# Optimization experiments

Measured on AMD Instinct MI355X. Metric: run time of the kernel, lower is better.

Reference implementation:

```python
import jax, jax.numpy as jnp
import numpy as np

L = 64          # latent_gcn == latent2_gcn == latent_linear
N = 8           # coarse_size (forward hardcodes eye(8))
NEG = 0.2       # LeakyReLU slope
EPS = 1e-5      # BatchNorm1d eps


def _bn(v, g, b):
    # training-mode BatchNorm1d over the node axis (axis=-2), per (B,C) instance
    m = v.mean(axis=-2, keepdims=True)
    var = ((v - m) ** 2).mean(axis=-2, keepdims=True)  # biased, as torch BN
    return (v - m) / jnp.sqrt(var + EPS) * g + b


def _path(A, W1, b1, W2, b2, Wm, bm, gm, betam, Ws, bs, gs, betas, noise):
    # A: [B, c, 8, 8] row-normalized adjacency. x = eye(8) so support1 = W1.
    x1 = jax.nn.leaky_relu(A @ W1 + b1, NEG)            # [B,c,8,L]
    x2 = jax.nn.leaky_relu(A @ (x1 @ W2) + b2, NEG)     # [B,c,8,L]
    mean = _bn(x2 @ Wm + bm, gm, betam)
    logvar = _bn(x2 @ Ws + bs, gs, betas)
    return mean + jnp.exp(0.5 * logvar) * noise         # reparameterization


def setup_inputs() -> dict:
    key = jax.random.key(0)
    ks = jax.random.split(key, 40)
    B, C = 2048, 32
    d = {
        "adj": jax.random.uniform(ks[0], (B, C, N, N), jnp.float32),
        "noise": jax.random.normal(ks[1], (N, L), jnp.float32),
    }
    i = 2
    for p in ("p", "n"):
        shapes = [
            (f"W1_{p}", (N, L)), (f"b1_{p}", (L,)),
            (f"W2_{p}", (L, L)), (f"b2_{p}", (L,)),
            (f"Wm_{p}", (L, L)), (f"bm_{p}", (L,)), (f"gm_{p}", (L,)), (f"betam_{p}", (L,)),
            (f"Ws_{p}", (L, L)), (f"bs_{p}", (L,)), (f"gs_{p}", (L,)), (f"betas_{p}", (L,)),
        ]
        for name, sh in shapes:
            if name.startswith("beta"):
                d[name] = jnp.zeros(sh, jnp.float32)
            elif name.startswith("g"):
                d[name] = jnp.ones(sh, jnp.float32)
            else:
                stdv = 1.0 / float(np.sqrt(sh[-1]))
                d[name] = jax.random.uniform(ks[i], sh, jnp.float32, -stdv, stdv)
                i += 1
    return d


def reference(adj, noise,
              W1_p, b1_p, W2_p, b2_p, Wm_p, bm_p, gm_p, betam_p, Ws_p, bs_p, gs_p, betas_p,
              W1_n, b1_n, W2_n, b2_n, Wm_n, bm_n, gm_n, betam_n, Ws_n, bs_n, gs_n, betas_n):
    # row-normalize each 8x8 adjacency (pygcn-style normalize)
    s = adj.sum(axis=-1, keepdims=True)
    A = adj / jnp.where(s == 0, 1.0, s)
    out_p = _path(A[:, :1], W1_p, b1_p, W2_p, b2_p, Wm_p, bm_p, gm_p, betam_p,
                  Ws_p, bs_p, gs_p, betas_p, noise)          # ii == 0
    out_n = _path(A[:, 1:], W1_n, b1_n, W2_n, b2_n, Wm_n, bm_n, gm_n, betam_n,
                  Ws_n, bs_n, gs_n, betas_n, noise)          # ii >= 1
    return jnp.concatenate([out_p, out_n], axis=1)           # [B, C, 8, L]
```

## Files before the change

### kernel.cpp

```cpp
#include <hip/hip_runtime.h>

typedef float v4f __attribute__((ext_vector_type(4)));
typedef short v8s __attribute__((ext_vector_type(8)));
typedef v8s v8s_a __attribute__((may_alias));

#define PBLOCKS 256
#define NEG 0.2f

static __device__ __forceinline__ void split8(const float* e, v8s& hi, v8s& lo) {
  union U { v8s s; unsigned u[4]; } H, L;
#pragma unroll
  for (int j = 0; j < 4; ++j) {
    union { float f; unsigned u; } e0, e1, h0, h1, l0, l1;
    e0.f = e[2 * j]; e1.f = e[2 * j + 1];
    H.u[j] = __builtin_amdgcn_perm(e1.u, e0.u, 0x07060302u);
    h0.u = e0.u & 0xFFFF0000u; h1.u = e1.u & 0xFFFF0000u;
    l0.f = e0.f - h0.f; l1.f = e1.f - h1.f;
    L.u[j] = __builtin_amdgcn_perm(l1.u, l0.u, 0x07060302u);
  }
  hi = H.s; lo = L.s;
}

static __device__ __forceinline__ v8s rne8(const float* e) {
  union U { v8s s; unsigned u[4]; } H;
#pragma unroll
  for (int j = 0; j < 4; ++j) {
    union { float f; unsigned u; } e0, e1;
    e0.f = e[2 * j]; e1.f = e[2 * j + 1];
    const unsigned r0 = e0.u + 0x7FFFu + ((e0.u >> 16) & 1u);
    const unsigned r1 = e1.u + 0x7FFFu + ((e1.u >> 16) & 1u);
    H.u[j] = __builtin_amdgcn_perm(r1, r0, 0x07060302u);
  }
  return H.s;
}

__global__ __launch_bounds__(256, 1)
void enc_reg(const float* __restrict__ adj, const float* __restrict__ noise,
             const float* __restrict__ W1p, const float* __restrict__ b1p,
             const float* __restrict__ W2p, const float* __restrict__ b2p,
             const float* __restrict__ Wmp, const float* __restrict__ bmp,
             const float* __restrict__ gmp, const float* __restrict__ betamp,
             const float* __restrict__ Wsp, const float* __restrict__ bsp,
             const float* __restrict__ gsp, const float* __restrict__ betasp,
             const float* __restrict__ W1n, const float* __restrict__ b1n,
             const float* __restrict__ W2n, const float* __restrict__ b2n,
             const float* __restrict__ Wmn, const float* __restrict__ bmn,
             const float* __restrict__ gmn, const float* __restrict__ betamn,
             const float* __restrict__ Wsn, const float* __restrict__ bsn,
             const float* __restrict__ gsn, const float* __restrict__ betasn,
             float* __restrict__ out)
{
  __shared__ __align__(16) short fragWhi[24 * 512];
  __shared__ __align__(16) short fragW1hi[4 * 256 + 8];

  const int tid = threadIdx.x;
  const int l = tid & 63;
  const int w = tid >> 6;
  const int n = l & 15;
  const int g = l >> 4;

  const bool isp = (blockIdx.x < PBLOCKS);
  const int bip = isp ? (int)blockIdx.x : ((int)blockIdx.x - PBLOCKS);

  const float* W1 = isp ? W1p : W1n;   const float* B1 = isp ? b1p : b1n;
  const float* W2 = isp ? W2p : W2n;   const float* B2 = isp ? b2p : b2n;
  const float* WM = isp ? Wmp : Wmn;   const float* BM = isp ? bmp : bmn;
  const float* GM = isp ? gmp : gmn;   const float* BEM = isp ? betamp : betamn;
  const float* WS = isp ? Wsp : Wsn;   const float* BS = isp ? bsp : bsn;
  const float* GS = isp ? gsp : gsn;   const float* BES = isp ? betasp : betasn;

  const int gi = bip * 4 + w;
  int iA, iB;
  if (isp) {
    iA = gi * 64;
    iB = gi * 64 + 32;
  } else {
    const unsigned n0 = 2u * (unsigned)gi;
    const unsigned n1 = n0 + 1u;
    const unsigned q0 = n0 / 31u;
    const unsigned q1 = n1 / 31u;
    iA = (int)(q0 * 32u + 1u + (n0 - q0 * 31u));
    iB = (int)(q1 * 32u + 1u + (n1 - q1 * 31u));
  }

  const int instAdj = (n >> 3) ? iB : iA;
  const float4 a0 = *(const float4*)(adj + instAdj * 64 + (n & 7) * 8);
  const float4 a1 = *(const float4*)(adj + instAdj * 64 + (n & 7) * 8 + 4);

  for (int f = w; f < 28; f += 4) {
    if (f < 24) {
      const float* M = (f < 8) ? W2 : ((f < 16) ? WM : WS);
      const int r = f & 7;
      const int kt = r >> 2;
      const int cn = (r & 3) * 16 + n;
      float v[8];
#pragma unroll
      for (int j = 0; j < 8; ++j)
        v[j] = M[(kt * 32 + g * 8 + j) * 64 + cn];
      *(v8s_a*)&fragWhi[f * 512 + l * 8] = rne8(v);
    } else {
      const int ft = f - 24;
      if (g < 2) {
        float v[8];
#pragma unroll
        for (int j = 0; j < 8; ++j)
          v[j] = W1[j * 64 + ft * 16 + n];
        *(v8s_a*)&fragW1hi[ft * 256 + l * 8] = rne8(v);
      } else if (f == 24 && l == 32) {
        const v8s z = { 0, 0, 0, 0, 0, 0, 0, 0 };
        *(v8s_a*)&fragW1hi[1024] = z;
      }
    }
  }
  __syncthreads();

  v8s afh, afl;
  {
    float s = a0.x + a0.y + a0.z + a0.w + a1.x + a1.y + a1.z + a1.w;
    s = (s == 0.0f) ? 1.0f : s;
    const float rinv = (g == (n >> 3)) ? (1.0f / s) : 0.0f;
    float e[8];
    e[0] = a0.x * rinv; e[1] = a0.y * rinv; e[2] = a0.z * rinv; e[3] = a0.w * rinv;
    e[4] = a1.x * rinv; e[5] = a1.y * rinv; e[6] = a1.z * rinv; e[7] = a1.w * rinv;
    split8(e, afh, afl);
  }

  v4f x1t[4];
#pragma unroll
  for (int ft = 0; ft < 4; ++ft) {
    const int w1off = (g < 2) ? (ft * 256 + l * 8) : 1024;
    const v8s w1h = *(const v8s_a*)&fragW1hi[w1off];
    const float4 b14 = *(const float4*)&B1[ft * 16 + g * 4];
    v4f acc = { b14.x, b14.y, b14.z, b14.w };
    acc = __builtin_amdgcn_mfma_f32_16x16x32_bf16(w1h, afl, acc, 0, 0, 0);
    acc = __builtin_amdgcn_mfma_f32_16x16x32_bf16(w1h, afh, acc, 0, 0, 0);
#pragma unroll
    for (int q = 0; q < 4; ++q) acc[q] = fmaxf(acc[q], NEG * acc[q]);
    x1t[ft] = acc;
  }

  v8s xah[2], xal[2];
  {
    const int srcLo = ((g & 1) << 5) + n;
    const int srcHi = srcLo + 16;
#pragma unroll
    for (int kc = 0; kc < 2; ++kc) {
      float e[8];
#pragma unroll
      for (int j = 0; j < 4; ++j) {
        const float lo0 = __shfl(x1t[2 * kc][j], srcLo);
        const float lo1 = __shfl(x1t[2 * kc + 1][j], srcLo);
        const float hi0 = __shfl(x1t[2 * kc][j], srcHi);
        const float hi1 = __shfl(x1t[2 * kc + 1][j], srcHi);
        e[j]     = (g >> 1) ? lo1 : lo0;
        e[j + 4] = (g >> 1) ? hi1 : hi0;
      }
      split8(e, xah[kc], xal[kc]);
    }
  }

  v4f tC[4];
#pragma unroll
  for (int nt = 0; nt < 4; ++nt) {
    v4f acc = { 0.0f, 0.0f, 0.0f, 0.0f };
#pragma unroll
    for (int kc = 0; kc < 2; ++kc) {
      const v8s bh = *(const v8s_a*)&fragWhi[(kc * 4 + nt) * 512 + l * 8];
      acc = __builtin_amdgcn_mfma_f32_16x16x32_bf16(xal[kc], bh, acc, 0, 0, 0);
      acc = __builtin_amdgcn_mfma_f32_16x16x32_bf16(xah[kc], bh, acc, 0, 0, 0);
    }
    tC[nt] = acc;
  }

  v4f x2t[4];
  {
    const int sA = ((g & 1) << 5) + n;
    const int sB = sA + 16;
    const bool bval = (g < 2);
#pragma unroll
    for (int ft = 0; ft < 4; ++ft) {
      float e[8];
#pragma unroll
      for (int j = 0; j < 4; ++j) {
        const float v0 = __shfl(tC[ft][j], sA);
        const float v1 = __shfl(tC[ft][j], sB);
        e[j]     = bval ? v0 : 0.0f;
        e[j + 4] = bval ? v1 : 0.0f;
      }
      v8s th, tl;
      split8(e, th, tl);
      const float4 b24 = *(const float4*)&B2[ft * 16 + g * 4];
      v4f acc = { b24.x, b24.y, b24.z, b24.w };
      acc = __builtin_amdgcn_mfma_f32_16x16x32_bf16(tl, afh, acc, 0, 0, 0);
      acc = __builtin_amdgcn_mfma_f32_16x16x32_bf16(th, afl, acc, 0, 0, 0);
      acc = __builtin_amdgcn_mfma_f32_16x16x32_bf16(th, afh, acc, 0, 0, 0);
#pragma unroll
      for (int q = 0; q < 4; ++q) acc[q] = fmaxf(acc[q], NEG * acc[q]);
      x2t[ft] = acc;
    }
  }

  v8s yah[2], yal[2];
  {
    const int srcLo = ((g & 1) << 5) + n;
    const int srcHi = srcLo + 16;
#pragma unroll
    for (int kc = 0; kc < 2; ++kc) {
      float e[8];
#pragma unroll
      for (int j = 0; j < 4; ++j) {
        const float lo0 = __shfl(x2t[2 * kc][j], srcLo);
        const float lo1 = __shfl(x2t[2 * kc + 1][j], srcLo);
        const float hi0 = __shfl(x2t[2 * kc][j], srcHi);
        const float hi1 = __shfl(x2t[2 * kc + 1][j], srcHi);
        e[j]     = (g >> 1) ? lo1 : lo0;
        e[j + 4] = (g >> 1) ? hi1 : hi0;
      }
      split8(e, yah[kc], yal[kc]);
    }
  }

  const int obase0 = ((g >> 1) ? iB : iA) * 512 + (g & 1) * 256;
#pragma unroll
  for (int nt = 0; nt < 4; ++nt) {
    const int cn = nt * 16 + n;
    v4f mc;
    {
      const float bm0 = BM[cn];
      mc[0] = bm0; mc[1] = bm0; mc[2] = bm0; mc[3] = bm0;
      const v8s bh0 = *(const v8s_a*)&fragWhi[(8 + nt) * 512 + l * 8];
      const v8s bh1 = *(const v8s_a*)&fragWhi[(12 + nt) * 512 + l * 8];
      mc = __builtin_amdgcn_mfma_f32_16x16x32_bf16(yal[0], bh0, mc, 0, 0, 0);
      mc = __builtin_amdgcn_mfma_f32_16x16x32_bf16(yah[0], bh0, mc, 0, 0, 0);
      mc = __builtin_amdgcn_mfma_f32_16x16x32_bf16(yal[1], bh1, mc, 0, 0, 0);
      mc = __builtin_amdgcn_mfma_f32_16x16x32_bf16(yah[1], bh1, mc, 0, 0, 0);
    }
    v4f sc;
    {
      const float bs0 = BS[cn];
      sc[0] = bs0; sc[1] = bs0; sc[2] = bs0; sc[3] = bs0;
      const v8s bh0 = *(const v8s_a*)&fragWhi[(16 + nt) * 512 + l * 8];
      const v8s bh1 = *(const v8s_a*)&fragWhi[(20 + nt) * 512 + l * 8];
      sc = __builtin_amdgcn_mfma_f32_16x16x32_bf16(yal[0], bh0, sc, 0, 0, 0);
      sc = __builtin_amdgcn_mfma_f32_16x16x32_bf16(yah[0], bh0, sc, 0, 0, 0);
      sc = __builtin_amdgcn_mfma_f32_16x16x32_bf16(yal[1], bh1, sc, 0, 0, 0);
      sc = __builtin_amdgcn_mfma_f32_16x16x32_bf16(yah[1], bh1, sc, 0, 0, 0);
    }

    float smm = (mc[0] + mc[1]) + (mc[2] + mc[3]);
    smm += __shfl_xor(smm, 16);
    const float mum = smm * 0.125f;
    float sms = (sc[0] + sc[1]) + (sc[2] + sc[3]);
    sms += __shfl_xor(sms, 16);
    const float mus = sms * 0.125f;
    float vm = 0.0f, vs = 0.0f;
#pragma unroll
    for (int q = 0; q < 4; ++q) {
      const float dm = mc[q] - mum; vm = fmaf(dm, dm, vm);
      const float ds = sc[q] - mus; vs = fmaf(ds, ds, vs);
    }
    vm += __shfl_xor(vm, 16);
    vs += __shfl_xor(vs, 16);
    const float sclm = GM[cn] * rsqrtf(vm * 0.125f + 1e-5f);
    const float scls = GS[cn] * rsqrtf(vs * 0.125f + 1e-5f);
    const float bem = BEM[cn];
    const float bes = BES[cn];
    const int oc = obase0 + cn;
#pragma unroll
    for (int q = 0; q < 4; ++q) {
      const float nzq = noise[((g & 1) * 4 + q) * 64 + cn];
      const float lv = (sc[q] - mus) * scls + bes;
      const float ex = exp2f(0.72134752044448f * lv);
      out[oc + q * 64] = (mc[q] - mum) * sclm + bem + ex * nzq;
    }
  }
}

extern "C" void kernel_launch(void* const* d_in, const int* in_sizes, int n_in,
                              void* d_out, int out_size, void* d_ws, size_t ws_size,
                              hipStream_t stream) {
  const float* adj   = (const float*)d_in[0];
  const float* noise = (const float*)d_in[1];
  const float* W1p = (const float*)d_in[2];  const float* b1p = (const float*)d_in[3];
  const float* W2p = (const float*)d_in[4];  const float* b2p = (const float*)d_in[5];
  const float* Wmp = (const float*)d_in[6];  const float* bmp = (const float*)d_in[7];
  const float* gmp = (const float*)d_in[8];  const float* betamp = (const float*)d_in[9];
  const float* Wsp = (const float*)d_in[10]; const float* bsp = (const float*)d_in[11];
  const float* gsp = (const float*)d_in[12]; const float* betasp = (const float*)d_in[13];
  const float* W1n = (const float*)d_in[14]; const float* b1n = (const float*)d_in[15];
  const float* W2n = (const float*)d_in[16]; const float* b2n = (const float*)d_in[17];
  const float* Wmn = (const float*)d_in[18]; const float* bmn = (const float*)d_in[19];
  const float* gmn = (const float*)d_in[20]; const float* betamn = (const float*)d_in[21];
  const float* Wsn = (const float*)d_in[22]; const float* bsn = (const float*)d_in[23];
  const float* gsn = (const float*)d_in[24]; const float* betasn = (const float*)d_in[25];

  enc_reg<<<8192, 256, 0, stream>>>(
      adj, noise,
      W1p, b1p, W2p, b2p, Wmp, bmp, gmp, betamp, Wsp, bsp, gsp, betasp,
      W1n, b1n, W2n, b2n, Wmn, bmn, gmn, betamn, Wsn, bsn, gsn, betasn,
      (float*)d_out);
}
```

Measured before the change: 88.49 us.

## Precompute bf16 weight fragments once in a prep kernel, read from global

Adds a small two-block prep kernel that converts W1/W2/Wm/Ws into bf16 MFMA fragment layout in workspace once per call. The main kernel drops its per-block gather, conversion, LDS staging and __syncthreads, and instead loads fragments directly from global memory, which should hit L2/L1 cache. This removes redundant per-block weight preprocessing across 8192 blocks, at the cost of an extra launch and global rather than LDS loads inside the MFMA loops.

```diff
diff --git a/kernel.cpp b/kernel.cpp
--- a/kernel.cpp
+++ b/kernel.cpp
@@ -35,24 +35,59 @@
 }
 
 __global__ __launch_bounds__(256, 1)
+void prep_frags(const float* __restrict__ W1p, const float* __restrict__ W2p,
+                const float* __restrict__ WMp, const float* __restrict__ WSp,
+                const float* __restrict__ W1n, const float* __restrict__ W2n,
+                const float* __restrict__ WMn, const float* __restrict__ WSn,
+                short* __restrict__ ws)
+{
+  const bool isp = (blockIdx.x == 0);
+  const float* W1 = isp ? W1p : W1n;
+  const float* W2 = isp ? W2p : W2n;
+  const float* WM = isp ? WMp : WMn;
+  const float* WS = isp ? WSp : WSn;
+  short* dst = ws + blockIdx.x * 28 * 512;
+
+  const int l = threadIdx.x & 63;
+  const int w = threadIdx.x >> 6;
+  const int n = l & 15;
+  const int g = l >> 4;
+
+  for (int f = w; f < 28; f += 4) {
+    float v[8];
+    if (f < 24) {
+      const float* M = (f < 8) ? W2 : ((f < 16) ? WM : WS);
+      const int r = f & 7;
+      const int kt = r >> 2;
+      const int cn = (r & 3) * 16 + n;
+#pragma unroll
+      for (int j = 0; j < 8; ++j)
+        v[j] = M[(kt * 32 + g * 8 + j) * 64 + cn];
+    } else {
+      const int ft = f - 24;
+#pragma unroll
+      for (int j = 0; j < 8; ++j)
+        v[j] = (g < 2) ? W1[j * 64 + ft * 16 + n] : 0.0f;
+    }
+    *(v8s_a*)&dst[f * 512 + l * 8] = rne8(v);
+  }
+}
+
+__global__ __launch_bounds__(256, 1)
 void enc_reg(const float* __restrict__ adj, const float* __restrict__ noise,
-             const float* __restrict__ W1p, const float* __restrict__ b1p,
-             const float* __restrict__ W2p, const float* __restrict__ b2p,
-             const float* __restrict__ Wmp, const float* __restrict__ bmp,
-             const float* __restrict__ gmp, const float* __restrict__ betamp,
-             const float* __restrict__ Wsp, const float* __restrict__ bsp,
-             const float* __restrict__ gsp, const float* __restrict__ betasp,
-             const float* __restrict__ W1n, const float* __restrict__ b1n,
-             const float* __restrict__ W2n, const float* __restrict__ b2n,
-             const float* __restrict__ Wmn, const float* __restrict__ bmn,
-             const float* __restrict__ gmn, const float* __restrict__ betamn,
-             const float* __restrict__ Wsn, const float* __restrict__ bsn,
-             const float* __restrict__ gsn, const float* __restrict__ betasn,
+             const short* __restrict__ ws,
+             const float* __restrict__ b1p, const float* __restrict__ b2p,
+             const float* __restrict__ bmp, const float* __restrict__ gmp,
+             const float* __restrict__ betamp,
+             const float* __restrict__ bsp, const float* __restrict__ gsp,
+             const float* __restrict__ betasp,
+             const float* __restrict__ b1n, const float* __restrict__ b2n,
+             const float* __restrict__ bmn, const float* __restrict__ gmn,
+             const float* __restrict__ betamn,
+             const float* __restrict__ bsn, const float* __restrict__ gsn,
+             const float* __restrict__ betasn,
              float* __restrict__ out)
 {
-  __shared__ __align__(16) short fragWhi[24 * 512];
-  __shared__ __align__(16) short fragW1hi[4 * 256 + 8];
-
   const int tid = threadIdx.x;
   const int l = tid & 63;
   const int w = tid >> 6;
@@ -62,12 +97,12 @@
   const bool isp = (blockIdx.x < PBLOCKS);
   const int bip = isp ? (int)blockIdx.x : ((int)blockIdx.x - PBLOCKS);
 
-  const float* W1 = isp ? W1p : W1n;   const float* B1 = isp ? b1p : b1n;
-  const float* W2 = isp ? W2p : W2n;   const float* B2 = isp ? b2p : b2n;
-  const float* WM = isp ? Wmp : Wmn;   const float* BM = isp ? bmp : bmn;
-  const float* GM = isp ? gmp : gmn;   const float* BEM = isp ? betamp : betamn;
-  const float* WS = isp ? Wsp : Wsn;   const float* BS = isp ? bsp : bsn;
-  const float* GS = isp ? gsp : gsn;   const float* BES = isp ? betasp : betasn;
+  const float* B1 = isp ? b1p : b1n;   const float* B2 = isp ? b2p : b2n;
+  const float* BM = isp ? bmp : bmn;   const float* GM = isp ? gmp : gmn;
+  const float* BEM = isp ? betamp : betamn;
+  const float* BS = isp ? bsp : bsn;   const float* GS = isp ? gsp : gsn;
+  const float* BES = isp ? betasp : betasn;
+  const short* fw = ws + (isp ? 0 : 1) * 28 * 512;
 
   const int gi = bip * 4 + w;
   int iA, iB;
@@ -83,39 +118,11 @@
     iB = (int)(q1 * 32u + 1u + (n1 - q1 * 31u));
   }
 
-  const int instAdj = (n >> 3) ? iB : iA;
-  const float4 a0 = *(const float4*)(adj + instAdj * 64 + (n & 7) * 8);
-  const float4 a1 = *(const float4*)(adj + instAdj * 64 + (n & 7) * 8 + 4);
-
-  for (int f = w; f < 28; f += 4) {
-    if (f < 24) {
-      const float* M = (f < 8) ? W2 : ((f < 16) ? WM : WS);
-      const int r = f & 7;
-      const int kt = r >> 2;
-      const int cn = (r & 3) * 16 + n;
-      float v[8];
-#pragma unroll
-      for (int j = 0; j < 8; ++j)
-        v[j] = M[(kt * 32 + g * 8 + j) * 64 + cn];
-      *(v8s_a*)&fragWhi[f * 512 + l * 8] = rne8(v);
-    } else {
-      const int ft = f - 24;
-      if (g < 2) {
-        float v[8];
-#pragma unroll
-        for (int j = 0; j < 8; ++j)
-          v[j] = W1[j * 64 + ft * 16 + n];
-        *(v8s_a*)&fragW1hi[ft * 256 + l * 8] = rne8(v);
-      } else if (f == 24 && l == 32) {
-        const v8s z = { 0, 0, 0, 0, 0, 0, 0, 0 };
-        *(v8s_a*)&fragW1hi[1024] = z;
-      }
-    }
-  }
-  __syncthreads();
-
   v8s afh, afl;
   {
+    const int instAdj = (n >> 3) ? iB : iA;
+    const float4 a0 = *(const float4*)(adj + instAdj * 64 + (n & 7) * 8);
+    const float4 a1 = *(const float4*)(adj + instAdj * 64 + (n & 7) * 8 + 4);
     float s = a0.x + a0.y + a0.z + a0.w + a1.x + a1.y + a1.z + a1.w;
     s = (s == 0.0f) ? 1.0f : s;
     const float rinv = (g == (n >> 3)) ? (1.0f / s) : 0.0f;
@@ -128,8 +135,7 @@
   v4f x1t[4];
 #pragma unroll
   for (int ft = 0; ft < 4; ++ft) {
-    const int w1off = (g < 2) ? (ft * 256 + l * 8) : 1024;
-    const v8s w1h = *(const v8s_a*)&fragW1hi[w1off];
+    const v8s w1h = *(const v8s_a*)&fw[(24 + ft) * 512 + l * 8];
     const float4 b14 = *(const float4*)&B1[ft * 16 + g * 4];
     v4f acc = { b14.x, b14.y, b14.z, b14.w };
     acc = __builtin_amdgcn_mfma_f32_16x16x32_bf16(w1h, afl, acc, 0, 0, 0);
@@ -165,7 +171,7 @@
     v4f acc = { 0.0f, 0.0f, 0.0f, 0.0f };
 #pragma unroll
     for (int kc = 0; kc < 2; ++kc) {
-      const v8s bh = *(const v8s_a*)&fragWhi[(kc * 4 + nt) * 512 + l * 8];
+      const v8s bh = *(const v8s_a*)&fw[(kc * 4 + nt) * 512 + l * 8];
       acc = __builtin_amdgcn_mfma_f32_16x16x32_bf16(xal[kc], bh, acc, 0, 0, 0);
       acc = __builtin_amdgcn_mfma_f32_16x16x32_bf16(xah[kc], bh, acc, 0, 0, 0);
     }
@@ -228,8 +234,8 @@
     {
       const float bm0 = BM[cn];
       mc[0] = bm0; mc[1] = bm0; mc[2] = bm0; mc[3] = bm0;
-      const v8s bh0 = *(const v8s_a*)&fragWhi[(8 + nt) * 512 + l * 8];
-      const v8s bh1 = *(const v8s_a*)&fragWhi[(12 + nt) * 512 + l * 8];
+      const v8s bh0 = *(const v8s_a*)&fw[(8 + nt) * 512 + l * 8];
+      const v8s bh1 = *(const v8s_a*)&fw[(12 + nt) * 512 + l * 8];
       mc = __builtin_amdgcn_mfma_f32_16x16x32_bf16(yal[0], bh0, mc, 0, 0, 0);
       mc = __builtin_amdgcn_mfma_f32_16x16x32_bf16(yah[0], bh0, mc, 0, 0, 0);
       mc = __builtin_amdgcn_mfma_f32_16x16x32_bf16(yal[1], bh1, mc, 0, 0, 0);
@@ -239,8 +245,8 @@
     {
       const float bs0 = BS[cn];
       sc[0] = bs0; sc[1] = bs0; sc[2] = bs0; sc[3] = bs0;
-      const v8s bh0 = *(const v8s_a*)&fragWhi[(16 + nt) * 512 + l * 8];
-      const v8s bh1 = *(const v8s_a*)&fragWhi[(20 + nt) * 512 + l * 8];
+      const v8s bh0 = *(const v8s_a*)&fw[(16 + nt) * 512 + l * 8];
+      const v8s bh1 = *(const v8s_a*)&fw[(20 + nt) * 512 + l * 8];
       sc = __builtin_amdgcn_mfma_f32_16x16x32_bf16(yal[0], bh0, sc, 0, 0, 0);
       sc = __builtin_amdgcn_mfma_f32_16x16x32_bf16(yah[0], bh0, sc, 0, 0, 0);
       sc = __builtin_amdgcn_mfma_f32_16x16x32_bf16(yal[1], bh1, sc, 0, 0, 0);
@@ -294,9 +300,13 @@
   const float* Wsn = (const float*)d_in[22]; const float* bsn = (const float*)d_in[23];
   const float* gsn = (const float*)d_in[24]; const float* betasn = (const float*)d_in[25];
 
+  short* ws = (short*)d_ws;
+
+  prep_frags<<<2, 256, 0, stream>>>(W1p, W2p, Wmp, Wsp, W1n, W2n, Wmn, Wsn, ws);
+
   enc_reg<<<8192, 256, 0, stream>>>(
-      adj, noise,
-      W1p, b1p, W2p, b2p, Wmp, bmp, gmp, betamp, Wsp, bsp, gsp, betasp,
-      W1n, b1n, W2n, b2n, Wmn, bmn, gmn, betamn, Wsn, bsn, gsn, betasn,
+      adj, noise, ws,
+      b1p, b2p, bmp, gmp, betamp, bsp, gsp, betasp,
+      b1n, b2n, bmn, gmn, betamn, bsn, gsn, betasn,
       (float*)d_out);
 }
```

Result: faster. 79.44 us (median of 2 runs) (-10.2%).
